# Kernel tuning notes

Measured on AMD Instinct MI355X. Metric: run time of the kernel, lower is better.

Reference implementation:

```python
import jax, jax.numpy as jnp
import numpy as np

N_NODES = 100000
N_EDGES = 1600000

def setup_inputs() -> dict:
    key = jax.random.key(0)
    ks = jax.random.split(key, 6)
    x = jax.random.normal(ks[0], (N_NODES, 128), dtype=jnp.float32)
    edge_index = jax.random.randint(ks[1], (2, N_EDGES), 0, N_NODES, dtype=jnp.int64)
    edge_weight = jax.random.uniform(ks[2], (N_EDGES,), dtype=jnp.float32)
    # kaiming-uniform-like init for weights, zeros for biases (as in reset_parameters)
    bound1 = float(np.sqrt(6.0 / 128))
    W1 = jax.random.uniform(ks[3], (128, 128), minval=-bound1, maxval=bound1, dtype=jnp.float32)
    b1 = jnp.zeros((128,), dtype=jnp.float32)
    W2 = jax.random.uniform(ks[4], (128, 64), minval=-bound1, maxval=bound1, dtype=jnp.float32)
    b2 = jnp.zeros((64,), dtype=jnp.float32)
    return {"x": x, "edge_index": edge_index, "edge_weight": edge_weight,
            "W1": W1, "b1": b1, "W2": W2, "b2": b2}

def _gcn_conv(x, src, dst, ew, W, b):
    support = x @ W                      # [N, F_out] dense GEMM
    msgs = ew[:, None] * support[src]    # [E, F_out] gather + scale (spmm values)
    out = jax.ops.segment_sum(msgs, dst, num_segments=N_NODES)  # scatter-add
    return out + b

def reference(x, edge_index, edge_weight, W1, b1, W2, b2):
    dst, src = edge_index[0], edge_index[1]  # adj[dst, src] = edge_weight
    h = _gcn_conv(x, src, dst, edge_weight, W1, b1)
    h = jax.nn.relu(h)
    out = _gcn_conv(h, src, dst, edge_weight, W2, b2)
    return out
```

## Files before the change

### kernel.cpp

```cpp
#include <hip/hip_runtime.h>

#define N_NODES 100000
#define N_EDGES 1600000
#define NB 391
#define PAD 16
#define SC_EPB 4096
#define SC_BLOCKS ((N_EDGES + SC_EPB - 1) / SC_EPB)
#define LDA 136
#define NTILES ((N_NODES + 127) / 128)
#define GEMM_BLOCKS 261

#define XQ_SCALE (5.5f / 127.0f)
#define XQ_INV   (127.0f / 5.5f)

#define PREP_X_BLOCKS ((N_NODES * 32 + 255) / 256)
#define PREP_W_BLOCKS 48
#define PREP_H_BLOCKS NB

typedef unsigned int uint32;
typedef __attribute__((ext_vector_type(8))) short bf16x8;
typedef __attribute__((ext_vector_type(4))) float f32x4;

__device__ __forceinline__ uint32 bf16_rne(float f) {
    uint32 u = __float_as_uint(f);
    return (u + 0x7fffu + ((u >> 16) & 1u)) >> 16;
}
__device__ __forceinline__ uint32 pack_bf16x2(float lo, float hi) {
    return bf16_rne(lo) | (bf16_rne(hi) << 16);
}
__device__ __forceinline__ float bf16_lo(uint32 u) { return __uint_as_float(u << 16); }
__device__ __forceinline__ float bf16_hi(uint32 u) { return __uint_as_float(u & 0xFFFF0000u); }

__device__ __forceinline__ float ub0(uint32 u) { return (float)(u & 255u); }
__device__ __forceinline__ float ub1(uint32 u) { return (float)((u >> 8) & 255u); }
__device__ __forceinline__ float ub2(uint32 u) { return (float)((u >> 16) & 255u); }
__device__ __forceinline__ float ub3(uint32 u) { return (float)(u >> 24); }

__device__ __forceinline__ uint32 q8(float v, float inv) {
    return (uint32)((int)rintf(fminf(fmaxf(v * inv, -127.f), 127.f)) + 128);
}

__global__ __launch_bounds__(256) void prep(const float* __restrict__ x,
                                            const float* __restrict__ W1,
                                            const float* __restrict__ W2,
                                            const int* __restrict__ dst,
                                            uint32* __restrict__ xq,
                                            uint32* __restrict__ w1tb,
                                            uint32* __restrict__ w2tb,
                                            int* __restrict__ bktCnt) {
    const int b = blockIdx.x;
    if (b < PREP_X_BLOCKS) {
        const int t = b * 256 + threadIdx.x;
        if (t >= N_NODES * 32) return;
        const float4 v = ((const float4*)x)[t];
        xq[t] = q8(v.x, XQ_INV) | (q8(v.y, XQ_INV) << 8)
              | (q8(v.z, XQ_INV) << 16) | (q8(v.w, XQ_INV) << 24);
    } else if (b < PREP_X_BLOCKS + PREP_W_BLOCKS) {
        const int t = (b - PREP_X_BLOCKS) * 256 + threadIdx.x;
        if (t < 128 * 64) {
            const int n = t >> 6, kk = t & 63;
            w1tb[t] = pack_bf16x2(W1[(2 * kk) * 128 + n], W1[(2 * kk + 1) * 128 + n]);
        } else if (t < 128 * 64 + 64 * 64) {
            const int u = t - 128 * 64;
            const int n = u >> 6, kk = u & 63;
            w2tb[u] = pack_bf16x2(W2[(2 * kk) * 64 + n], W2[(2 * kk + 1) * 64 + n]);
        }
    } else {
        __shared__ int h[NB];
        const int bh = b - PREP_X_BLOCKS - PREP_W_BLOCKS;
        for (int i = threadIdx.x; i < NB; i += 256) h[i] = 0;
        __syncthreads();
        for (int e = bh * 256 + threadIdx.x; e < N_EDGES; e += NB * 256)
            atomicAdd(&h[dst[e] >> 8], 1);
        __syncthreads();
        for (int i = threadIdx.x; i < NB; i += 256)
            if (h[i]) atomicAdd(&bktCnt[i * PAD], h[i]);
    }
}

__global__ __launch_bounds__(512) void bucket_scatter2(const int* __restrict__ dst,
                                                       const int* __restrict__ src,
                                                       const float* __restrict__ ew,
                                                       const int* __restrict__ bktCnt,
                                                       int* __restrict__ bCur,
                                                       int2* __restrict__ bucketed) {
    __shared__ int h[NB];
    __shared__ int cur[NB];
    __shared__ int s[512];
    const int t    = threadIdx.x;
    const int base = blockIdx.x * SC_EPB;
    const int end  = min(base + SC_EPB, N_EDGES);

    for (int i = t; i < NB; i += 512) h[i] = 0;
    __syncthreads();
    for (int e = base + t; e < end; e += 512)
        atomicAdd(&h[dst[e] >> 8], 1);
    __syncthreads();

    const int v = (t < NB) ? bktCnt[t * PAD] : 0;
    s[t] = v;
    __syncthreads();
#pragma unroll
    for (int off = 1; off < 512; off <<= 1) {
        const int u = (t >= off) ? s[t - off] : 0;
        __syncthreads();
        s[t] += u;
        __syncthreads();
    }
    if (t < NB) {
        const int c = h[t];
        cur[t] = (s[t] - v) + (c ? atomicAdd(&bCur[t * PAD], c) : 0);
    }
    __syncthreads();
    for (int e = base + t; e < end; e += 512) {
        const int d = dst[e];
        const int p = atomicAdd(&cur[d >> 8], 1);
        bucketed[p] = make_int2(src[e] | ((d & 255) << 17), __float_as_int(ew[e]));
    }
}

__global__ __launch_bounds__(512) void bucket_csr(const int2* __restrict__ bucketed,
                                                  const int* __restrict__ bktCnt,
                                                  int* __restrict__ offs,
                                                  int2* __restrict__ csr_ef) {
    __shared__ int sdeg[256];
    __shared__ int lcur[256];
    __shared__ int red[512];
    __shared__ int s_beg, s_end;
    const int b = blockIdx.x;
    const int t = threadIdx.x;

    int partial = 0;
    for (int k = t; k < b; k += 512) partial += bktCnt[k * PAD];
    red[t] = partial;
    __syncthreads();
#pragma unroll
    for (int off = 256; off > 0; off >>= 1) {
        if (t < off) red[t] += red[t + off];
        __syncthreads();
    }
    if (t == 0) {
        s_beg = red[0];
        s_end = red[0] + bktCnt[b * PAD];
        if (b == 0) offs[N_NODES] = N_EDGES;
    }
    if (t < 256) sdeg[t] = 0;
    __syncthreads();
    const int beg = s_beg, end = s_end;

    for (int j = beg + t; j < end; j += 512)
        atomicAdd(&sdeg[(bucketed[j].x >> 17) & 255], 1);
    __syncthreads();
    const int mydeg = (t < 256) ? sdeg[t] : 0;
#pragma unroll
    for (int off = 1; off < 256; off <<= 1) {
        const int u = (t >= off && t < 256) ? sdeg[t - off] : 0;
        __syncthreads();
        if (t < 256) sdeg[t] += u;
        __syncthreads();
    }
    if (t < 256) {
        const int excl = sdeg[t] - mydeg;
        lcur[t] = excl;
        const int node = b * 256 + t;
        if (node < N_NODES) offs[node] = beg + excl;
    }
    __syncthreads();

    for (int j = beg + t; j < end; j += 512) {
        const int2 v = bucketed[j];
        const int dl = (v.x >> 17) & 255;
        const int p  = beg + atomicAdd(&lcur[dl], 1);
        csr_ef[p] = make_int2(v.x & 0x1FFFF, v.y);
    }
}

template <int FEAT>
__global__ __launch_bounds__(256) void aggregate(const void* __restrict__ featv,
                                                 const int* __restrict__ offs,
                                                 const int2* __restrict__ csr_ef,
                                                 const float* __restrict__ bias,
                                                 void* __restrict__ outv) {
    const int n    = (blockIdx.x * 256 + threadIdx.x) >> 6;
    const int lane = threadIdx.x & 63;
    if (n >= N_NODES) return;
    const int beg = offs[n], end = offs[n + 1];
    const uint2* feat = (const uint2*)featv;

    const int g = lane >> 4;
    const int f = lane & 15;

    if constexpr (FEAT == 128) {
        float u0 = 0.f, u1 = 0.f, u2 = 0.f, u3 = 0.f;
        float u4 = 0.f, u5 = 0.f, u6 = 0.f, u7 = 0.f;
        float wsum = 0.f;

        for (int j = beg + g; j < end; j += 8) {
#pragma unroll
            for (int uu = 0; uu < 2; ++uu) {
                const int jj = j + uu * 4;
                if (uu == 0 || jj < end) {
                    const int2 e = csr_ef[jj];
                    const uint2 r = feat[(unsigned)(e.x * 16 + f)];
                    const float w = __int_as_float(e.y);
                    wsum += w;
                    u0 += w * ub0(r.x); u1 += w * ub1(r.x);
                    u2 += w * ub2(r.x); u3 += w * ub3(r.x);
                    u4 += w * ub0(r.y); u5 += w * ub1(r.y);
                    u6 += w * ub2(r.y); u7 += w * ub3(r.y);
                }
            }
        }

#pragma unroll
        for (int d = 16; d < 64; d <<= 1) {
            u0 += __shfl_xor(u0, d); u1 += __shfl_xor(u1, d);
            u2 += __shfl_xor(u2, d); u3 += __shfl_xor(u3, d);
            u4 += __shfl_xor(u4, d); u5 += __shfl_xor(u5, d);
            u6 += __shfl_xor(u6, d); u7 += __shfl_xor(u7, d);
            wsum += __shfl_xor(wsum, d);
        }

        if (g == 0) {
            const float off128 = 128.f * wsum;
            const float s = XQ_SCALE;
            uint4 p;
            p.x = pack_bf16x2(s * (u0 - off128), s * (u1 - off128));
            p.y = pack_bf16x2(s * (u2 - off128), s * (u3 - off128));
            p.z = pack_bf16x2(s * (u4 - off128), s * (u5 - off128));
            p.w = pack_bf16x2(s * (u6 - off128), s * (u7 - off128));
            ((uint4*)outv)[(size_t)n * 16 + f] = p;
        }
    } else {
        float a0 = 0.f, a1 = 0.f, a2 = 0.f, a3 = 0.f;

        for (int j = beg + g; j < end; j += 8) {
#pragma unroll
            for (int uu = 0; uu < 2; ++uu) {
                const int jj = j + uu * 4;
                if (uu == 0 || jj < end) {
                    const int2 e = csr_ef[jj];
                    const uint2 r = feat[(unsigned)(e.x * 16 + f)];
                    const float w = __int_as_float(e.y);
                    a0 += w * bf16_lo(r.x); a1 += w * bf16_hi(r.x);
                    a2 += w * bf16_lo(r.y); a3 += w * bf16_hi(r.y);
                }
            }
        }

#pragma unroll
        for (int d = 16; d < 64; d <<= 1) {
            a0 += __shfl_xor(a0, d); a1 += __shfl_xor(a1, d);
            a2 += __shfl_xor(a2, d); a3 += __shfl_xor(a3, d);
        }

        if (g == 0) {
            const float4 bb = ((const float4*)bias)[f];
            ((float4*)outv)[(size_t)n * 16 + f] =
                make_float4(a0 + bb.x, a1 + bb.y, a2 + bb.z, a3 + bb.w);
        }
    }
}

__global__ __launch_bounds__(512) void gemm_fused(const uint32* __restrict__ aggPb,
                                                  const uint32* __restrict__ w1tb,
                                                  const float* __restrict__ b1,
                                                  const uint32* __restrict__ w2tb,
                                                  uint32* __restrict__ sup2b, int N) {
    __shared__ __align__(16) short As[128 * LDA];
    __shared__ __align__(16) short W1s[128 * LDA];
    __shared__ __align__(16) short W2s[64 * LDA];
    __shared__ __align__(16) short Ts[128 * LDA];

    const int tid = threadIdx.x;

    for (int i = tid; i < 128 * 16; i += 512)
        *(uint4*)&W1s[(i >> 4) * LDA + (i & 15) * 8] = ((const uint4*)w1tb)[i];
    for (int i = tid; i < 64 * 16; i += 512)
        *(uint4*)&W2s[(i >> 4) * LDA + (i & 15) * 8] = ((const uint4*)w2tb)[i];

    const int wave = tid >> 6;
    const int lane = tid & 63;
    const int m    = lane & 15;
    const int quad = lane >> 4;
    const int rowbase = (wave & 3) * 32;
    const int colbase = (wave >> 2) * 64;

    float b1r[4];
#pragma unroll
    for (int ct = 0; ct < 4; ++ct) b1r[ct] = b1[colbase + ct * 16 + m];

    for (int tile = blockIdx.x; tile < NTILES; tile += gridDim.x) {
        const int row0 = tile * 128;
        __syncthreads();

#pragma unroll
        for (int i = 0; i < 4; ++i) {
            const int idx = i * 512 + tid;
            const int row = idx >> 4, c4 = idx & 15;
            const int grow = row0 + row;
            uint4 v = make_uint4(0u, 0u, 0u, 0u);
            if (grow < N) v = ((const uint4*)aggPb)[(size_t)grow * 16 + c4];
            *(uint4*)&As[row * LDA + c4 * 8] = v;
        }
        __syncthreads();

        bf16x8 afrag[2][4];
#pragma unroll
        for (int ss = 0; ss < 2; ++ss)
#pragma unroll
            for (int ch = 0; ch < 4; ++ch)
                afrag[ss][ch] = *(const bf16x8*)&As[(rowbase + ss * 16 + m) * LDA + ch * 32 + quad * 8];

        f32x4 acc[2][4];
#pragma unroll
        for (int ss = 0; ss < 2; ++ss)
#pragma unroll
            for (int ct = 0; ct < 4; ++ct) acc[ss][ct] = (f32x4){0.f, 0.f, 0.f, 0.f};

#pragma unroll
        for (int ct = 0; ct < 4; ++ct) {
            bf16x8 bfr[4];
#pragma unroll
            for (int ch = 0; ch < 4; ++ch)
                bfr[ch] = *(const bf16x8*)&W1s[(colbase + ct * 16 + m) * LDA + ch * 32 + quad * 8];
#pragma unroll
            for (int ss = 0; ss < 2; ++ss)
#pragma unroll
                for (int ch = 0; ch < 4; ++ch)
                    acc[ss][ct] = __builtin_amdgcn_mfma_f32_16x16x32_bf16(
                        afrag[ss][ch], bfr[ch], acc[ss][ct], 0, 0, 0);
        }

#pragma unroll
        for (int ss = 0; ss < 2; ++ss)
#pragma unroll
            for (int ct = 0; ct < 4; ++ct)
#pragma unroll
                for (int r = 0; r < 4; ++r) {
                    const float v = fmaxf(acc[ss][ct][r] + b1r[ct], 0.f);
                    const int row = rowbase + ss * 16 + quad * 4 + r;
                    const int col = colbase + ct * 16 + m;
                    Ts[row * LDA + col] = (short)bf16_rne(v);
                }
        __syncthreads();

        const int rb2 = wave * 16;
        bf16x8 tfrag[4];
#pragma unroll
        for (int ch = 0; ch < 4; ++ch)
            tfrag[ch] = *(const bf16x8*)&Ts[(rb2 + m) * LDA + ch * 32 + quad * 8];

        f32x4 acc2[4];
#pragma unroll
        for (int ct = 0; ct < 4; ++ct) acc2[ct] = (f32x4){0.f, 0.f, 0.f, 0.f};
#pragma unroll
        for (int ct = 0; ct < 4; ++ct)
#pragma unroll
            for (int ch = 0; ch < 4; ++ch) {
                const bf16x8 bfr = *(const bf16x8*)&W2s[(ct * 16 + m) * LDA + ch * 32 + quad * 8];
                acc2[ct] = __builtin_amdgcn_mfma_f32_16x16x32_bf16(
                    tfrag[ch], bfr, acc2[ct], 0, 0, 0);
            }

#pragma unroll
        for (int ct = 0; ct < 4; ++ct)
#pragma unroll
            for (int r = 0; r < 4; ++r) {
                const int row = rb2 + quad * 4 + r;
                const int col = ct * 16 + m;
                As[row * LDA + col] = (short)bf16_rne(acc2[ct][r]);
            }
        __syncthreads();
#pragma unroll
        for (int i = 0; i < 2; ++i) {
            const int idx = i * 512 + tid;
            const int row = idx >> 3, c4 = idx & 7;
            if (row0 + row < N)
                ((uint4*)sup2b)[(size_t)(row0 + row) * 8 + c4] = *(uint4*)&As[row * LDA + c4 * 8];
        }
    }
}

extern "C" void kernel_launch(void* const* d_in, const int* in_sizes, int n_in,
                              void* d_out, int out_size, void* d_ws, size_t ws_size,
                              hipStream_t stream) {
    const float* x  = (const float*)d_in[0];
    const int*   ei = (const int*)d_in[1];
    const float* ew = (const float*)d_in[2];
    const float* W1 = (const float*)d_in[3];
    const float* b1 = (const float*)d_in[4];
    const float* W2 = (const float*)d_in[5];
    const float* b2 = (const float*)d_in[6];
    float* out = (float*)d_out;

    const int* dstIdx = ei;
    const int* srcIdx = ei + N_EDGES;

    uint32* xb      = (uint32*)d_ws;
    uint32* aggPb   = xb + (size_t)N_NODES * 64;
    uint32* w1tb    = aggPb + (size_t)N_NODES * 64;
    uint32* w2tb    = w1tb + 128 * 64;
    int2*   csr_ef  = (int2*)(xb + (size_t)N_NODES * 192);
    int*    bktCnt  = (int*)(csr_ef + N_EDGES);
    int*    bCur    = bktCnt + NB * PAD;
    int*    offs    = bCur + NB * PAD;
    int2*   bucketed = (int2*)aggPb;
    uint32* sup2b   = xb;

    (void)hipMemsetAsync(bktCnt, 0, (size_t)2 * NB * PAD * sizeof(int), stream);

    prep<<<PREP_X_BLOCKS + PREP_W_BLOCKS + PREP_H_BLOCKS, 256, 0, stream>>>(
        x, W1, W2, dstIdx, xb, w1tb, w2tb, bktCnt);

    bucket_scatter2<<<SC_BLOCKS, 512, 0, stream>>>(dstIdx, srcIdx, ew, bktCnt,
                                                   bCur, bucketed);
    bucket_csr<<<NB, 512, 0, stream>>>(bucketed, bktCnt, offs, csr_ef);

    aggregate<128><<<(N_NODES * 64) / 256, 256, 0, stream>>>(xb, offs, csr_ef,
                                                             nullptr, aggPb);
    gemm_fused<<<GEMM_BLOCKS, 512, 0, stream>>>(aggPb, w1tb, b1, w2tb, sup2b, N_NODES);

    aggregate<64><<<(N_NODES * 64) / 256, 256, 0, stream>>>(sup2b, offs, csr_ef,
                                                            b2, out);
}
```

Before: 318.7 us.

## Merge prep, bucket scatter and CSR build into one cooperative kernel

Replaces the memset and the three separate preprocessing launches (quantize/weight pack/histogram, bucket scatter, per-bucket CSR) with one cooperative kernel that uses grid-wide syncs between phases. It also reuses the block-level prefix scan from the scatter phase as the bucket base, so the CSR phase no longer re-reduces the bucket counts. The aim is to cut launch overhead and inter-kernel gaps. In exchange the grid is fixed at 391 blocks of 512 threads, which must all be co-resident, and the x-quantize phase has less parallelism. The GEMM block count also changes from 261 to 256.

```diff
diff --git a/kernel.cpp b/kernel.cpp
--- a/kernel.cpp
+++ b/kernel.cpp
@@ -1,21 +1,23 @@
 #include <hip/hip_runtime.h>
+#include <hip/hip_cooperative_groups.h>
+
+namespace cg = cooperative_groups;
 
 #define N_NODES 100000
 #define N_EDGES 1600000
 #define NB 391
 #define PAD 16
 #define SC_EPB 4096
-#define SC_BLOCKS ((N_EDGES + SC_EPB - 1) / SC_EPB)
 #define LDA 136
 #define NTILES ((N_NODES + 127) / 128)
-#define GEMM_BLOCKS 261
+#define GEMM_BLOCKS 256
+
+#define CB_BLOCKS NB
+#define CB_THREADS 512
+#define CB_GT (CB_BLOCKS * CB_THREADS)
 
 #define XQ_SCALE (5.5f / 127.0f)
 #define XQ_INV   (127.0f / 5.5f)
-
-#define PREP_X_BLOCKS ((N_NODES * 32 + 255) / 256)
-#define PREP_W_BLOCKS 48
-#define PREP_H_BLOCKS NB
 
 typedef unsigned int uint32;
 typedef __attribute__((ext_vector_type(8))) short bf16x8;
@@ -40,115 +42,97 @@
     return (uint32)((int)rintf(fminf(fmaxf(v * inv, -127.f), 127.f)) + 128);
 }
 
-__global__ __launch_bounds__(256) void prep(const float* __restrict__ x,
-                                            const float* __restrict__ W1,
-                                            const float* __restrict__ W2,
-                                            const int* __restrict__ dst,
-                                            uint32* __restrict__ xq,
-                                            uint32* __restrict__ w1tb,
-                                            uint32* __restrict__ w2tb,
-                                            int* __restrict__ bktCnt) {
-    const int b = blockIdx.x;
-    if (b < PREP_X_BLOCKS) {
-        const int t = b * 256 + threadIdx.x;
-        if (t >= N_NODES * 32) return;
-        const float4 v = ((const float4*)x)[t];
-        xq[t] = q8(v.x, XQ_INV) | (q8(v.y, XQ_INV) << 8)
+__global__ __launch_bounds__(CB_THREADS) void coop_build(
+        const float* __restrict__ x,
+        const float* __restrict__ W1,
+        const float* __restrict__ W2,
+        const int* __restrict__ dst,
+        const int* __restrict__ src,
+        const float* __restrict__ ew,
+        uint32* __restrict__ xq,
+        uint32* __restrict__ w1tb,
+        uint32* __restrict__ w2tb,
+        int* __restrict__ bktCnt,
+        int2* __restrict__ bucketed,
+        int* __restrict__ offs,
+        int2* __restrict__ csr_ef) {
+    cg::grid_group grid = cg::this_grid();
+
+    __shared__ int h[NB];
+    __shared__ int cur[NB];
+    __shared__ int sbase[NB];
+    __shared__ int s[CB_THREADS];
+    __shared__ int sdeg[256];
+    __shared__ int lcur[256];
+
+    const int t  = threadIdx.x;
+    const int b  = blockIdx.x;
+    const int gt = b * CB_THREADS + t;
+    int* bCur = bktCnt + NB * PAD;
+
+    for (int i = gt; i < 2 * NB * PAD; i += CB_GT) bktCnt[i] = 0;
+    for (int i = gt; i < N_NODES * 32; i += CB_GT) {
+        const float4 v = ((const float4*)x)[i];
+        xq[i] = q8(v.x, XQ_INV) | (q8(v.y, XQ_INV) << 8)
               | (q8(v.z, XQ_INV) << 16) | (q8(v.w, XQ_INV) << 24);
-    } else if (b < PREP_X_BLOCKS + PREP_W_BLOCKS) {
-        const int t = (b - PREP_X_BLOCKS) * 256 + threadIdx.x;
-        if (t < 128 * 64) {
-            const int n = t >> 6, kk = t & 63;
-            w1tb[t] = pack_bf16x2(W1[(2 * kk) * 128 + n], W1[(2 * kk + 1) * 128 + n]);
-        } else if (t < 128 * 64 + 64 * 64) {
-            const int u = t - 128 * 64;
+    }
+    for (int i = gt; i < 128 * 64 + 64 * 64; i += CB_GT) {
+        if (i < 128 * 64) {
+            const int n = i >> 6, kk = i & 63;
+            w1tb[i] = pack_bf16x2(W1[(2 * kk) * 128 + n], W1[(2 * kk + 1) * 128 + n]);
+        } else {
+            const int u = i - 128 * 64;
             const int n = u >> 6, kk = u & 63;
             w2tb[u] = pack_bf16x2(W2[(2 * kk) * 64 + n], W2[(2 * kk + 1) * 64 + n]);
         }
-    } else {
-        __shared__ int h[NB];
-        const int bh = b - PREP_X_BLOCKS - PREP_W_BLOCKS;
-        for (int i = threadIdx.x; i < NB; i += 256) h[i] = 0;
-        __syncthreads();
-        for (int e = bh * 256 + threadIdx.x; e < N_EDGES; e += NB * 256)
-            atomicAdd(&h[dst[e] >> 8], 1);
-        __syncthreads();
-        for (int i = threadIdx.x; i < NB; i += 256)
-            if (h[i]) atomicAdd(&bktCnt[i * PAD], h[i]);
-    }
-}
-
-__global__ __launch_bounds__(512) void bucket_scatter2(const int* __restrict__ dst,
-                                                       const int* __restrict__ src,
-                                                       const float* __restrict__ ew,
-                                                       const int* __restrict__ bktCnt,
-                                                       int* __restrict__ bCur,
-                                                       int2* __restrict__ bucketed) {
-    __shared__ int h[NB];
-    __shared__ int cur[NB];
-    __shared__ int s[512];
-    const int t    = threadIdx.x;
-    const int base = blockIdx.x * SC_EPB;
+    }
+    grid.sync();
+
+    for (int i = t; i < NB; i += CB_THREADS) h[i] = 0;
+    __syncthreads();
+    for (int e = gt; e < N_EDGES; e += CB_GT)
+        atomicAdd(&h[dst[e] >> 8], 1);
+    __syncthreads();
+    for (int i = t; i < NB; i += CB_THREADS)
+        if (h[i]) atomicAdd(&bktCnt[i * PAD], h[i]);
+    grid.sync();
+
+    for (int i = t; i < NB; i += CB_THREADS) h[i] = 0;
+    __syncthreads();
+    const int base = b * SC_EPB;
     const int end  = min(base + SC_EPB, N_EDGES);
-
-    for (int i = t; i < NB; i += 512) h[i] = 0;
-    __syncthreads();
-    for (int e = base + t; e < end; e += 512)
+    for (int e = base + t; e < end; e += CB_THREADS)
         atomicAdd(&h[dst[e] >> 8], 1);
     __syncthreads();
-
     const int v = (t < NB) ? bktCnt[t * PAD] : 0;
     s[t] = v;
     __syncthreads();
 #pragma unroll
-    for (int off = 1; off < 512; off <<= 1) {
+    for (int off = 1; off < CB_THREADS; off <<= 1) {
         const int u = (t >= off) ? s[t - off] : 0;
         __syncthreads();
         s[t] += u;
         __syncthreads();
     }
     if (t < NB) {
+        sbase[t] = s[t] - v;
         const int c = h[t];
         cur[t] = (s[t] - v) + (c ? atomicAdd(&bCur[t * PAD], c) : 0);
     }
     __syncthreads();
-    for (int e = base + t; e < end; e += 512) {
+    for (int e = base + t; e < end; e += CB_THREADS) {
         const int d = dst[e];
         const int p = atomicAdd(&cur[d >> 8], 1);
         bucketed[p] = make_int2(src[e] | ((d & 255) << 17), __float_as_int(ew[e]));
     }
-}
-
-__global__ __launch_bounds__(512) void bucket_csr(const int2* __restrict__ bucketed,
-                                                  const int* __restrict__ bktCnt,
-                                                  int* __restrict__ offs,
-                                                  int2* __restrict__ csr_ef) {
-    __shared__ int sdeg[256];
-    __shared__ int lcur[256];
-    __shared__ int red[512];
-    __shared__ int s_beg, s_end;
-    const int b = blockIdx.x;
-    const int t = threadIdx.x;
-
-    int partial = 0;
-    for (int k = t; k < b; k += 512) partial += bktCnt[k * PAD];
-    red[t] = partial;
-    __syncthreads();
-#pragma unroll
-    for (int off = 256; off > 0; off >>= 1) {
-        if (t < off) red[t] += red[t + off];
-        __syncthreads();
-    }
-    if (t == 0) {
-        s_beg = red[0];
-        s_end = red[0] + bktCnt[b * PAD];
-        if (b == 0) offs[N_NODES] = N_EDGES;
-    }
+    grid.sync();
+
+    const int beg3 = sbase[b];
+    const int end3 = beg3 + bktCnt[b * PAD];
     if (t < 256) sdeg[t] = 0;
-    __syncthreads();
-    const int beg = s_beg, end = s_end;
-
-    for (int j = beg + t; j < end; j += 512)
+    if (t == 0 && b == 0) offs[N_NODES] = N_EDGES;
+    __syncthreads();
+    for (int j = beg3 + t; j < end3; j += CB_THREADS)
         atomicAdd(&sdeg[(bucketed[j].x >> 17) & 255], 1);
     __syncthreads();
     const int mydeg = (t < 256) ? sdeg[t] : 0;
@@ -163,15 +147,14 @@
         const int excl = sdeg[t] - mydeg;
         lcur[t] = excl;
         const int node = b * 256 + t;
-        if (node < N_NODES) offs[node] = beg + excl;
-    }
-    __syncthreads();
-
-    for (int j = beg + t; j < end; j += 512) {
-        const int2 v = bucketed[j];
-        const int dl = (v.x >> 17) & 255;
-        const int p  = beg + atomicAdd(&lcur[dl], 1);
-        csr_ef[p] = make_int2(v.x & 0x1FFFF, v.y);
+        if (node < N_NODES) offs[node] = beg3 + excl;
+    }
+    __syncthreads();
+    for (int j = beg3 + t; j < end3; j += CB_THREADS) {
+        const int2 vv = bucketed[j];
+        const int dl = (vv.x >> 17) & 255;
+        const int p  = beg3 + atomicAdd(&lcur[dl], 1);
+        csr_ef[p] = make_int2(vv.x & 0x1FFFF, vv.y);
     }
 }
 
@@ -403,19 +386,18 @@
     uint32* w2tb    = w1tb + 128 * 64;
     int2*   csr_ef  = (int2*)(xb + (size_t)N_NODES * 192);
     int*    bktCnt  = (int*)(csr_ef + N_EDGES);
-    int*    bCur    = bktCnt + NB * PAD;
-    int*    offs    = bCur + NB * PAD;
+    int*    offs    = bktCnt + 2 * NB * PAD;
     int2*   bucketed = (int2*)aggPb;
     uint32* sup2b   = xb;
 
-    (void)hipMemsetAsync(bktCnt, 0, (size_t)2 * NB * PAD * sizeof(int), stream);
-
-    prep<<<PREP_X_BLOCKS + PREP_W_BLOCKS + PREP_H_BLOCKS, 256, 0, stream>>>(
-        x, W1, W2, dstIdx, xb, w1tb, w2tb, bktCnt);
-
-    bucket_scatter2<<<SC_BLOCKS, 512, 0, stream>>>(dstIdx, srcIdx, ew, bktCnt,
-                                                   bCur, bucketed);
-    bucket_csr<<<NB, 512, 0, stream>>>(bucketed, bktCnt, offs, csr_ef);
+    void* cb_args[] = {
+        (void*)&x, (void*)&W1, (void*)&W2,
+        (void*)&dstIdx, (void*)&srcIdx, (void*)&ew,
+        (void*)&xb, (void*)&w1tb, (void*)&w2tb,
+        (void*)&bktCnt, (void*)&bucketed, (void*)&offs, (void*)&csr_ef
+    };
+    (void)hipLaunchCooperativeKernel((void*)coop_build, dim3(CB_BLOCKS),
+                                     dim3(CB_THREADS), cb_args, 0, stream);
 
     aggregate<128><<<(N_NODES * 64) / 256, 256, 0, stream>>>(xb, offs, csr_ef,
                                                              nullptr, aggPb);
```

Result: slower. 470.8 us (+47.7%).
